# Kernel optimization log

Hardware: AMD Instinct MI355X
Metric: run time of the kernel (lower is better)

The kernel has to match this reference:

```python
import jax, jax.numpy as jnp
import numpy as np

N = 16384          # tokens
D_IN = 512         # input_dim
D_OUT = 512        # output_dim
H = 256            # expert hidden
E = 10             # num_experts
TOP_K = 2


def setup_inputs() -> dict:
    key = jax.random.key(0)
    ks = jax.random.split(key, 12)
    s_in = 1.0 / np.sqrt(D_IN)
    s_h = 1.0 / np.sqrt(H)
    s_o = 1.0 / np.sqrt(D_OUT)
    return {
        "x": jax.random.normal(ks[0], (N, D_IN), dtype=jnp.float32),
        "gate_w": jax.random.uniform(ks[1], (D_IN, E), minval=-s_in, maxval=s_in),
        "gate_b": jax.random.uniform(ks[2], (E,), minval=-s_in, maxval=s_in),
        "w1": jax.random.uniform(ks[3], (E, D_IN, H), minval=-s_in, maxval=s_in),
        "b1": jax.random.uniform(ks[4], (E, H), minval=-s_in, maxval=s_in),
        "w2": jax.random.uniform(ks[5], (E, H, D_OUT), minval=-s_h, maxval=s_h),
        "b2": jax.random.uniform(ks[6], (E, D_OUT), minval=-s_h, maxval=s_h),
        "cls_w": jax.random.uniform(ks[7], (D_OUT, D_OUT), minval=-s_o, maxval=s_o),
        "cls_b": jax.random.uniform(ks[8], (D_OUT,), minval=-s_o, maxval=s_o),
        "vec_w": jax.random.uniform(ks[9], (D_OUT, D_OUT), minval=-s_o, maxval=s_o),
        "vec_b": jax.random.uniform(ks[10], (D_OUT,), minval=-s_o, maxval=s_o),
    }


def reference(x, gate_w, gate_b, w1, b1, w2, b2, cls_w, cls_b, vec_w, vec_b):
    # Gating: softmax over experts, take top-k, renormalize
    gate_probs = jax.nn.softmax(x @ gate_w + gate_b, axis=-1)          # [N, E]
    top_v, top_i = jax.lax.top_k(gate_probs, TOP_K)                    # [N, K]
    top_v = top_v / jnp.sum(top_v, axis=-1, keepdims=True)
    # Scatter renormalized top-k probs into dense per-expert weights [N, E]
    n_idx = jnp.arange(x.shape[0])[:, None]
    w = jnp.zeros_like(gate_probs).at[n_idx, top_i].add(top_v)
    # Expert MLPs (vectorized over experts; zero weight == not dispatched)
    h = jax.nn.relu(jnp.einsum("nd,edh->neh", x, w1) + b1)             # [N, E, H]
    y = jnp.einsum("neh,eho->neo", h, w2) + b2                          # [N, E, Dout]
    combined = jnp.einsum("neo,ne->no", y, w)                           # [N, Dout]
    cls_out = combined @ cls_w + cls_b
    vec_out = combined @ vec_w + vec_b
    return (cls_out, vec_out)
```

## Files before the change

### kernel.cpp

```cpp
#include <hip/hip_runtime.h>

#define NTOK 16384
#define DIN  512
#define DOUT 512
#define HDIM 256
#define NEXP 10
#define NSLOT (2*NTOK)
#define NSEG  (2*NEXP)
#define BM 128
#define BN 128
#define BK 64

typedef unsigned short u16;
typedef unsigned int   u32;
typedef short s16x8 __attribute__((ext_vector_type(8)));
typedef float f32x4 __attribute__((ext_vector_type(4)));

__device__ __forceinline__ u16 f2b(float f){
  union { float f; u32 u; } c; c.f = f;
  u32 r = c.u + 0x7FFFu + ((c.u >> 16) & 1u);
  return (u16)(r >> 16);
}
__device__ __forceinline__ float b2f(u16 v){
  union { u32 u; float f; } c; c.u = ((u32)v) << 16; return c.f;
}
__device__ __forceinline__ u32 pk2(float lo, float hi){
  return (u32)f2b(lo) | ((u32)f2b(hi) << 16);
}
__device__ __forceinline__ s16x8 cvt8(const float* p){
  f32x4 a = *(const f32x4*)p;
  f32x4 b = *(const f32x4*)(p + 4);
  s16x8 r;
  r[0]=(short)f2b(a[0]); r[1]=(short)f2b(a[1]); r[2]=(short)f2b(a[2]); r[3]=(short)f2b(a[3]);
  r[4]=(short)f2b(b[0]); r[5]=(short)f2b(b[1]); r[6]=(short)f2b(b[2]); r[7]=(short)f2b(b[3]);
  return r;
}

__global__ __launch_bounds__(64) void k_zero(int* counts){
  if (threadIdx.x < NSEG) counts[threadIdx.x] = 0;
}

__global__ __launch_bounds__(256) void k_gate(
    const float* __restrict__ x, const float* __restrict__ gw, const float* __restrict__ gb,
    int* __restrict__ tke, float* __restrict__ tkw, int* __restrict__ counts)
{
  __shared__ int cnt[NSEG];
  if (threadIdx.x < NSEG) cnt[threadIdx.x] = 0;
  __syncthreads();
  const int wave = threadIdx.x >> 6, lane = threadIdx.x & 63;
  const int token = blockIdx.x * 4 + wave;
  float acc[NEXP];
  #pragma unroll
  for (int e = 0; e < NEXP; ++e) acc[e] = 0.f;
  const float* xr = x + (size_t)token * DIN;
  #pragma unroll
  for (int i = 0; i < DIN/64; ++i){
    int d = lane + 64*i;
    float xv = xr[d];
    const float* g = gw + (size_t)d * NEXP;
    #pragma unroll
    for (int e = 0; e < NEXP; ++e) acc[e] += xv * g[e];
  }
  #pragma unroll
  for (int e = 0; e < NEXP; ++e){
    #pragma unroll
    for (int off = 32; off > 0; off >>= 1) acc[e] += __shfl_xor(acc[e], off, 64);
  }
  if (lane == 0){
    float l[NEXP];
    #pragma unroll
    for (int e = 0; e < NEXP; ++e) l[e] = acc[e] + gb[e];
    int bi = 0; float bv = l[0];
    #pragma unroll
    for (int e = 1; e < NEXP; ++e) if (l[e] > bv){ bv = l[e]; bi = e; }
    int si = -1; float sv = -1e30f;
    #pragma unroll
    for (int e = 0; e < NEXP; ++e) if (e != bi && l[e] > sv){ sv = l[e]; si = e; }
    float w0 = 1.f / (1.f + expf(sv - bv));
    tke[2*token]   = bi;  tke[2*token+1] = si;
    tkw[2*token]   = w0;  tkw[2*token+1] = 1.f - w0;
    atomicAdd(&cnt[2*bi], 1);  atomicAdd(&cnt[2*si+1], 1);
  }
  __syncthreads();
  if (threadIdx.x < NSEG && cnt[threadIdx.x] > 0)
    atomicAdd(&counts[threadIdx.x], cnt[threadIdx.x]);
}

__global__ __launch_bounds__(64) void k_scan(
    const int* __restrict__ counts, int* __restrict__ offsets, int* __restrict__ cursors)
{
  if (threadIdx.x == 0){
    int s = 0;
    for (int i = 0; i < NSEG; ++i){ offsets[i] = s; s += counts[i]; }
    offsets[NSEG] = s;
  }
  if (threadIdx.x < NSEG) cursors[threadIdx.x] = 0;
}

__global__ __launch_bounds__(256) void k_scatter(
    const int* __restrict__ tke, const float* __restrict__ tkw,
    const int* __restrict__ offsets, int* __restrict__ cursors,
    int* __restrict__ tok_slot, float* __restrict__ w_slot)
{
  __shared__ int lcnt[NSEG], lbase[NSEG];
  if (threadIdx.x < NSEG) lcnt[threadIdx.x] = 0;
  __syncthreads();
  int n = blockIdx.x * 256 + threadIdx.x;
  int g0 = 2*tke[2*n], g1 = 2*tke[2*n+1] + 1;
  int p0 = atomicAdd(&lcnt[g0], 1);
  int p1 = atomicAdd(&lcnt[g1], 1);
  __syncthreads();
  if (threadIdx.x < NSEG) lbase[threadIdx.x] = atomicAdd(&cursors[threadIdx.x], lcnt[threadIdx.x]);
  __syncthreads();
  int s0 = offsets[g0] + lbase[g0] + p0;
  int s1 = offsets[g1] + lbase[g1] + p1;
  tok_slot[s0] = n; w_slot[s0] = tkw[2*n];
  tok_slot[s1] = n; w_slot[s1] = tkw[2*n+1];
}

__global__ __launch_bounds__(256) void k_wt(
    const float* __restrict__ in, u16* __restrict__ out, int R, int C)
{
  __shared__ float tile[32][33];
  const float* src = in + (size_t)blockIdx.z * R * C;
  u16* dst = out + (size_t)blockIdx.z * R * C;
  int cb = blockIdx.x * 32, rb = blockIdx.y * 32;
  int tx = threadIdx.x & 31, ty = threadIdx.x >> 5;
  #pragma unroll
  for (int i = 0; i < 4; ++i)
    tile[ty + i*8][tx] = src[(size_t)(rb + ty + i*8) * C + cb + tx];
  __syncthreads();
  #pragma unroll
  for (int i = 0; i < 4; ++i)
    dst[(size_t)(cb + ty + i*8) * R + rb + tx] = f2b(tile[tx][ty + i*8]);
}

__global__ __launch_bounds__(256, 2) void k_h(
    const float* __restrict__ x, const u16* __restrict__ w1tb, const float* __restrict__ b1,
    const int* __restrict__ offsets, const int* __restrict__ tok_slot,
    u16* __restrict__ h)
{
  __shared__ __align__(16) char pool[65536];
  u16* As = (u16*)pool;
  u16* Bs = (u16*)(pool + 32768);
  __shared__ int toks[BM];
  const int e   = blockIdx.z;
  const int off = offsets[2*e];
  const int cnt = offsets[2*e+2] - off;
  const int c0  = blockIdx.x * BM;
  if (c0 >= cnt) return;
  const int n0  = blockIdx.y * BN;
  const int tid = threadIdx.x;

  if (tid < BM){
    int r = c0 + tid;
    toks[tid] = tok_slot[off + (r < cnt ? r : cnt - 1)];
  }
  __syncthreads();

  const u16* Bg = w1tb + ((size_t)e * HDIM + n0) * DIN;

  int crow[4], ckk[4];
  #pragma unroll
  for (int i = 0; i < 4; ++i){
    int c = tid + i*256;
    crow[i] = c >> 3; ckk[i] = (c & 7) * 8;
  }
  int tokr[4];
  #pragma unroll
  for (int i = 0; i < 4; ++i) tokr[i] = toks[crow[i]];

  s16x8 ra[4], rb[4];
  auto loadregs = [&](int ks){
    #pragma unroll
    for (int i = 0; i < 4; ++i){
      ra[i] = cvt8(x + (size_t)tokr[i]*DIN + ks*BK + ckk[i]);
      rb[i] = *(const s16x8*)(Bg + (size_t)crow[i]*DIN + ks*BK + ckk[i]);
    }
  };
  auto writeregs = [&](int buf){
    #pragma unroll
    for (int i = 0; i < 4; ++i){
      u32 byt = (u32)((crow[i]*BK + ckk[i])*2) ^ ((u32)(crow[i]&7)<<4);
      *(s16x8*)((char*)As + buf*16384 + byt) = ra[i];
      *(s16x8*)((char*)Bs + buf*16384 + byt) = rb[i];
    }
  };

  const int wv = tid >> 6, lane = tid & 63;
  const int lr = lane & 15, lk = lane >> 4;
  const int wr = (wv >> 1) * 64, wc = (wv & 1) * 64;

  f32x4 acc[4][4];
  #pragma unroll
  for (int i = 0; i < 4; ++i)
    #pragma unroll
    for (int j = 0; j < 4; ++j) acc[i][j] = (f32x4){0.f,0.f,0.f,0.f};

  loadregs(0); writeregs(0);
  int cur = 0;
  const int NK = DIN / BK;
  for (int ks = 0; ks < NK; ++ks){
    __syncthreads();
    if (ks + 1 < NK) loadregs(ks + 1);
    #pragma unroll
    for (int sub = 0; sub < 2; ++sub){
      s16x8 af[4], bf[4];
      #pragma unroll
      for (int g = 0; g < 4; ++g){
        int arow = wr + g*16 + lr;
        u32 ab = (u32)((arow*BK + sub*32 + lk*8)*2) ^ ((u32)(arow&7)<<4);
        af[g] = *(const s16x8*)((char*)As + cur*16384 + ab);
        int bcol = wc + g*16 + lr;
        u32 bb = (u32)((bcol*BK + sub*32 + lk*8)*2) ^ ((u32)(bcol&7)<<4);
        bf[g] = *(const s16x8*)((char*)Bs + cur*16384 + bb);
      }
      #pragma unroll
      for (int i = 0; i < 4; ++i)
        #pragma unroll
        for (int j = 0; j < 4; ++j)
          acc[i][j] = __builtin_amdgcn_mfma_f32_16x16x32_bf16(af[i], bf[j], acc[i][j], 0, 0, 0);
    }
    if (ks + 1 < NK) writeregs(cur ^ 1);
    cur ^= 1;
  }
  __syncthreads();

  u16* outh = (u16*)pool;
  #pragma unroll
  for (int j = 0; j < 4; ++j){
    int col = wc + j*16 + lr;
    float bias = b1[e*HDIM + n0 + col];
    #pragma unroll
    for (int i = 0; i < 4; ++i)
      #pragma unroll
      for (int r = 0; r < 4; ++r){
        int row = wr + i*16 + lk*4 + r;
        float v = acc[i][j][r] + bias;
        outh[row*136 + col] = f2b(v > 0.f ? v : 0.f);
      }
  }
  __syncthreads();
  {
    int r = tid >> 1, half = tid & 1;
    if (c0 + r < cnt){
      u16* dst = h + (size_t)(off + c0 + r) * HDIM + n0 + half*64;
      const u16* src = outh + r*136 + half*64;
      #pragma unroll
      for (int q = 0; q < 8; ++q)
        *(s16x8*)(dst + q*8) = *(const s16x8*)(src + q*8);
    }
  }
}

template<int PASS>
__global__ __launch_bounds__(256, 2) void k_y(
    const u16* __restrict__ h, const u16* __restrict__ w2tb, const float* __restrict__ b2,
    const int* __restrict__ offsets, const int* __restrict__ tok_slot,
    const float* __restrict__ w_slot, u16* __restrict__ cmb)
{
  __shared__ __align__(16) char pool[67584];
  u16* As = (u16*)pool;
  u16* Bs = (u16*)(pool + 32768);
  __shared__ int   toks[BM];
  __shared__ float wts[BM];
  const int e    = blockIdx.z;
  const int segb = offsets[2*e + PASS];
  const int segc = offsets[2*e + PASS + 1] - segb;
  const int c0   = blockIdx.x * BM;
  if (c0 >= segc) return;
  const int n0   = blockIdx.y * BN;
  const int tid  = threadIdx.x;

  if (tid < BM){
    int r = c0 + tid;
    int s = segb + (r < segc ? r : segc - 1);
    toks[tid] = tok_slot[s];
    wts[tid]  = w_slot[s];
  }

  const u16* Ag = h + (size_t)(segb + c0) * HDIM;
  const u16* Bg = w2tb + ((size_t)e * DOUT + n0) * HDIM;

  int crow[4], ckk[4];
  #pragma unroll
  for (int i = 0; i < 4; ++i){
    int c = tid + i*256;
    crow[i] = c >> 3; ckk[i] = (c & 7) * 8;
  }
  s16x8 ra[4], rb[4];
  auto loadregs = [&](int ks){
    #pragma unroll
    for (int i = 0; i < 4; ++i){
      ra[i] = *(const s16x8*)(Ag + (size_t)crow[i]*HDIM + ks*BK + ckk[i]);
      rb[i] = *(const s16x8*)(Bg + (size_t)crow[i]*HDIM + ks*BK + ckk[i]);
    }
  };
  auto writeregs = [&](int buf){
    #pragma unroll
    for (int i = 0; i < 4; ++i){
      u32 byt = (u32)((crow[i]*BK + ckk[i])*2) ^ ((u32)(crow[i]&7)<<4);
      *(s16x8*)((char*)As + buf*16384 + byt) = ra[i];
      *(s16x8*)((char*)Bs + buf*16384 + byt) = rb[i];
    }
  };

  const int wv = tid >> 6, lane = tid & 63;
  const int lr = lane & 15, lk = lane >> 4;
  const int wr = (wv >> 1) * 64, wc = (wv & 1) * 64;

  f32x4 acc[4][4];
  #pragma unroll
  for (int i = 0; i < 4; ++i)
    #pragma unroll
    for (int j = 0; j < 4; ++j) acc[i][j] = (f32x4){0.f,0.f,0.f,0.f};

  loadregs(0); writeregs(0);
  int cur = 0;
  const int NK = HDIM / BK;
  for (int ks = 0; ks < NK; ++ks){
    __syncthreads();
    if (ks + 1 < NK) loadregs(ks + 1);
    #pragma unroll
    for (int sub = 0; sub < 2; ++sub){
      s16x8 af[4], bf[4];
      #pragma unroll
      for (int g = 0; g < 4; ++g){
        int arow = wr + g*16 + lr;
        u32 ab = (u32)((arow*BK + sub*32 + lk*8)*2) ^ ((u32)(arow&7)<<4);
        af[g] = *(const s16x8*)((char*)As + cur*16384 + ab);
        int bcol = wc + g*16 + lr;
        u32 bb = (u32)((bcol*BK + sub*32 + lk*8)*2) ^ ((u32)(bcol&7)<<4);
        bf[g] = *(const s16x8*)((char*)Bs + cur*16384 + bb);
      }
      #pragma unroll
      for (int i = 0; i < 4; ++i)
        #pragma unroll
        for (int j = 0; j < 4; ++j)
          acc[i][j] = __builtin_amdgcn_mfma_f32_16x16x32_bf16(af[i], bf[j], acc[i][j], 0, 0, 0);
    }
    if (ks + 1 < NK) writeregs(cur ^ 1);
    cur ^= 1;
  }
  __syncthreads();

  float* outf = (float*)pool;
  #pragma unroll
  for (int j = 0; j < 4; ++j){
    int col = wc + j*16 + lr;
    float bias = b2[e*DOUT + n0 + col];
    #pragma unroll
    for (int i = 0; i < 4; ++i)
      #pragma unroll
      for (int r = 0; r < 4; ++r){
        int row = wr + i*16 + lk*4 + r;
        outf[row*132 + col] = wts[row] * (acc[i][j][r] + bias);
      }
  }
  __syncthreads();
  {
    int r = tid >> 1, half = tid & 1;
    if (c0 + r < segc){
      u16* dst = cmb + (size_t)toks[r] * 1024 + n0 + half*64;
      const float* src = outf + r*132 + half*64;
      #pragma unroll
      for (int q = 0; q < 8; ++q){
        s16x8 o;
        if (PASS == 0){
          #pragma unroll
          for (int m = 0; m < 8; ++m) o[m] = (short)f2b(src[q*8 + m]);
        } else {
          s16x8 old = *(const s16x8*)(dst + q*8);
          #pragma unroll
          for (int m = 0; m < 8; ++m)
            o[m] = (short)f2b(b2f((u16)old[m]) + src[q*8 + m]);
        }
        *(s16x8*)(dst + q*8) = o;
      }
    }
  }
}

__global__ __launch_bounds__(512, 4) void k_cls(
    const u16* __restrict__ cmb, const float* __restrict__ W,
    const float* __restrict__ bias, float* __restrict__ out)
{
  __shared__ __align__(16) char Bs[2][10240];
  const int tid = threadIdx.x;
  const int r0  = blockIdx.x * 256;
  const int c0  = blockIdx.y * 128;

  const int bc4 = tid >> 4;
  const int bkp = tid & 15;
  u32 bpk[4];
  auto loadB = [&](int ks){
    const float* p0 = W + (size_t)(ks*32 + 2*bkp) * DOUT + c0 + bc4*4;
    f32x4 v0 = *(const f32x4*)p0;
    f32x4 v1 = *(const f32x4*)(p0 + DOUT);
    #pragma unroll
    for (int m = 0; m < 4; ++m) bpk[m] = pk2(v0[m], v1[m]);
  };
  auto writeB = [&](int buf){
    #pragma unroll
    for (int m = 0; m < 4; ++m)
      *(u32*)(Bs[buf] + (bc4*4 + m)*80 + bkp*4) = bpk[m];
  };

  const int wv = tid >> 6, lane = tid & 63;
  const int lr = lane & 15, lk = lane >> 4;
  const int rg = wv >> 1, cg = wv & 1;
  const u16* Arow = cmb + (size_t)(r0 + rg*64) * 1024;

  f32x4 acc[4][4];
  #pragma unroll
  for (int i = 0; i < 4; ++i)
    #pragma unroll
    for (int j = 0; j < 4; ++j) acc[i][j] = (f32x4){0.f,0.f,0.f,0.f};

  s16x8 af[4], afn[4];
  auto loadA = [&](s16x8* a, int ks){
    #pragma unroll
    for (int g = 0; g < 4; ++g)
      a[g] = *(const s16x8*)(Arow + (size_t)(g*16 + lr)*1024 + ks*32 + lk*8);
  };

  loadB(0); writeB(0); loadA(af, 0);
  int cur = 0;
  for (int ks = 0; ks < 16; ++ks){
    __syncthreads();
    if (ks + 1 < 16){ loadB(ks + 1); loadA(afn, ks + 1); }
    s16x8 bf[4];
    #pragma unroll
    for (int j = 0; j < 4; ++j)
      bf[j] = *(const s16x8*)(Bs[cur] + (cg*64 + j*16 + lr)*80 + lk*16);
    #pragma unroll
    for (int i = 0; i < 4; ++i)
      #pragma unroll
      for (int j = 0; j < 4; ++j)
        acc[i][j] = __builtin_amdgcn_mfma_f32_16x16x32_bf16(af[i], bf[j], acc[i][j], 0, 0, 0);
    if (ks + 1 < 16) writeB(cur ^ 1);
    #pragma unroll
    for (int g = 0; g < 4; ++g) af[g] = afn[g];
    cur ^= 1;
  }

  #pragma unroll
  for (int j = 0; j < 4; ++j){
    int col = c0 + cg*64 + j*16 + lr;
    float bv = bias[col];
    #pragma unroll
    for (int i = 0; i < 4; ++i)
      #pragma unroll
      for (int r = 0; r < 4; ++r){
        int row = r0 + rg*64 + i*16 + lk*4 + r;
        out[(size_t)row * DOUT + col] = acc[i][j][r] + bv;
      }
  }
}

__global__ __launch_bounds__(512, 2) void k_vip(
    const float* __restrict__ W, const float* __restrict__ bias,
    u16* __restrict__ cmbio)
{
  __shared__ __align__(16) char Bs[2][40960];
  const int tid = threadIdx.x;
  const int r0  = blockIdx.x * 64;

  int bc4[4], bkp[4];
  #pragma unroll
  for (int u = 0; u < 4; ++u){
    int idx = tid + u*512;
    bc4[u] = idx >> 4;
    bkp[u] = idx & 15;
  }
  u32 bpk[4][4];
  auto loadB = [&](int ks){
    #pragma unroll
    for (int u = 0; u < 4; ++u){
      const float* p0 = W + (size_t)(ks*32 + 2*bkp[u]) * DOUT + bc4[u]*4;
      f32x4 v0 = *(const f32x4*)p0;
      f32x4 v1 = *(const f32x4*)(p0 + DOUT);
      #pragma unroll
      for (int m = 0; m < 4; ++m) bpk[u][m] = pk2(v0[m], v1[m]);
    }
  };
  auto writeB = [&](int buf){
    #pragma unroll
    for (int u = 0; u < 4; ++u)
      #pragma unroll
      for (int m = 0; m < 4; ++m)
        *(u32*)(Bs[buf] + (bc4[u]*4 + m)*80 + bkp[u]*4) = bpk[u][m];
  };

  const int wv = tid >> 6, lane = tid & 63;
  const int lr = lane & 15, lk = lane >> 4;
  const int wc = wv * 64;
  const u16* Arow = cmbio + (size_t)r0 * 1024;

  f32x4 acc[4][4];
  #pragma unroll
  for (int i = 0; i < 4; ++i)
    #pragma unroll
    for (int j = 0; j < 4; ++j) acc[i][j] = (f32x4){0.f,0.f,0.f,0.f};

  s16x8 af[4], afn[4];
  auto loadA = [&](s16x8* a, int ks){
    #pragma unroll
    for (int g = 0; g < 4; ++g)
      a[g] = *(const s16x8*)(Arow + (size_t)(g*16 + lr)*1024 + ks*32 + lk*8);
  };

  loadB(0); writeB(0); loadA(af, 0);
  int cur = 0;
  for (int ks = 0; ks < 16; ++ks){
    __syncthreads();
    if (ks + 1 < 16){ loadB(ks + 1); loadA(afn, ks + 1); }
    s16x8 bf[4];
    #pragma unroll
    for (int g = 0; g < 4; ++g)
      bf[g] = *(const s16x8*)(Bs[cur] + (wc + g*16 + lr)*80 + lk*16);
    #pragma unroll
    for (int i = 0; i < 4; ++i)
      #pragma unroll
      for (int j = 0; j < 4; ++j)
        acc[i][j] = __builtin_amdgcn_mfma_f32_16x16x32_bf16(af[i], bf[j], acc[i][j], 0, 0, 0);
    if (ks + 1 < 16) writeB(cur ^ 1);
    #pragma unroll
    for (int g = 0; g < 4; ++g) af[g] = afn[g];
    cur ^= 1;
  }
  __syncthreads();

  float* out = (float*)cmbio;
  #pragma unroll
  for (int j = 0; j < 4; ++j){
    int col = wc + j*16 + lr;
    float bv = bias[col];
    #pragma unroll
    for (int i = 0; i < 4; ++i)
      #pragma unroll
      for (int r = 0; r < 4; ++r){
        int row = r0 + i*16 + lk*4 + r;
        out[(size_t)row * DOUT + col] = acc[i][j][r] + bv;
      }
  }
}

extern "C" void kernel_launch(void* const* d_in, const int* in_sizes, int n_in,
                              void* d_out, int out_size, void* d_ws, size_t ws_size,
                              hipStream_t stream)
{
  const float* x    = (const float*)d_in[0];
  const float* gw   = (const float*)d_in[1];
  const float* gb   = (const float*)d_in[2];
  const float* w1   = (const float*)d_in[3];
  const float* b1   = (const float*)d_in[4];
  const float* w2   = (const float*)d_in[5];
  const float* b2   = (const float*)d_in[6];
  const float* clsw = (const float*)d_in[7];
  const float* clsb = (const float*)d_in[8];
  const float* vecw = (const float*)d_in[9];
  const float* vecb = (const float*)d_in[10];

  char* base = (char*)d_out;
  float* cls_out  = (float*)base;
  u16*   cmb      = (u16*)(base + ((size_t)32<<20));
  u16*   h        = (u16*)base;
  char*  mb       = base + ((size_t)16<<20) + (128<<10);
  int*   tok_slot = (int*)  mb;
  float* w_slot   = (float*)(mb + 131072);
  int*   tke      = (int*)  (mb + 262144);
  float* tkw      = (float*)(mb + 393216);
  int*   counts   = (int*)  (mb + 524288);
  int*   offsets  = (int*)  (mb + 524544);
  int*   cursors  = (int*)  (mb + 524800);
  u16*   w1tb     = (u16*)(base + ((size_t)18<<20));
  u16*   w2tb     = (u16*)(base + ((size_t)21<<20));

  k_zero<<<dim3(1), dim3(64), 0, stream>>>(counts);
  k_gate<<<dim3(NTOK/4), dim3(256), 0, stream>>>(x, gw, gb, tke, tkw, counts);
  k_scan<<<dim3(1), dim3(64), 0, stream>>>(counts, offsets, cursors);
  k_scatter<<<dim3(NTOK/256), dim3(256), 0, stream>>>(tke, tkw, offsets, cursors,
                                                      tok_slot, w_slot);
  k_wt<<<dim3(HDIM/32, DIN/32, NEXP), dim3(256), 0, stream>>>(w1, w1tb, DIN, HDIM);
  k_wt<<<dim3(DOUT/32, HDIM/32, NEXP), dim3(256), 0, stream>>>(w2, w2tb, HDIM, DOUT);
  k_h<<<dim3(256, 2, NEXP), dim3(256), 0, stream>>>(x, w1tb, b1, offsets, tok_slot, h);
  k_y<0><<<dim3(128, 4, NEXP), dim3(256), 0, stream>>>(h, w2tb, b2, offsets, tok_slot, w_slot, cmb);
  k_y<1><<<dim3(128, 4, NEXP), dim3(256), 0, stream>>>(h, w2tb, b2, offsets, tok_slot, w_slot, cmb);
  k_cls<<<dim3(NTOK/256, DOUT/128), dim3(512), 0, stream>>>(cmb, clsw, clsb, cls_out);
  k_vip<<<dim3(NTOK/64), dim3(512), 0, stream>>>(vecw, vecb, cmb);
}
```

Measured before the change: 252.2 us.

## Pretranspose vec weights into workspace and use hardware bf16 pack conversion

Converts fp32 to bf16 with the v_cvt_pk_bf16_f32 instruction instead of manual bit rounding. When the workspace holds at least 1 MB, the vec_w matrix is pre-transposed into bf16 there. A new in-place kernel then reads its B fragments straight from global memory with no LDS staging, 32 rows per block. The goal is to cut conversion ALU work and the in-kernel weight conversion and LDS traffic in the final projection. The cost is an extra transpose launch and uncached, uncoalesced-ish global B loads.

```diff
diff --git a/kernel.cpp b/kernel.cpp
--- a/kernel.cpp
+++ b/kernel.cpp
@@ -25,15 +25,17 @@
   union { u32 u; float f; } c; c.u = ((u32)v) << 16; return c.f;
 }
 __device__ __forceinline__ u32 pk2(float lo, float hi){
-  return (u32)f2b(lo) | ((u32)f2b(hi) << 16);
+  u32 r;
+  asm("v_cvt_pk_bf16_f32 %0, %1, %2" : "=v"(r) : "v"(lo), "v"(hi));
+  return r;
 }
 __device__ __forceinline__ s16x8 cvt8(const float* p){
   f32x4 a = *(const f32x4*)p;
   f32x4 b = *(const f32x4*)(p + 4);
-  s16x8 r;
-  r[0]=(short)f2b(a[0]); r[1]=(short)f2b(a[1]); r[2]=(short)f2b(a[2]); r[3]=(short)f2b(a[3]);
-  r[4]=(short)f2b(b[0]); r[5]=(short)f2b(b[1]); r[6]=(short)f2b(b[2]); r[7]=(short)f2b(b[3]);
-  return r;
+  union { u32 u[4]; s16x8 v; } c;
+  c.u[0] = pk2(a[0], a[1]); c.u[1] = pk2(a[2], a[3]);
+  c.u[2] = pk2(b[0], b[1]); c.u[3] = pk2(b[2], b[3]);
+  return c.v;
 }
 
 __global__ __launch_bounds__(64) void k_zero(int* counts){
@@ -538,6 +540,53 @@
     float bv = bias[col];
     #pragma unroll
     for (int i = 0; i < 4; ++i)
+      #pragma unroll
+      for (int r = 0; r < 4; ++r){
+        int row = r0 + i*16 + lk*4 + r;
+        out[(size_t)row * DOUT + col] = acc[i][j][r] + bv;
+      }
+  }
+}
+
+__global__ __launch_bounds__(256, 4) void k_vipw(
+    const u16* __restrict__ wT, const float* __restrict__ bias,
+    u16* __restrict__ cmbio)
+{
+  const int tid = threadIdx.x;
+  const int r0  = blockIdx.x * 32;
+  const int wv = tid >> 6, lane = tid & 63;
+  const int lr = lane & 15, lk = lane >> 4;
+  const int wc = wv * 128;
+  const u16* Arow = cmbio + (size_t)r0 * 1024;
+
+  f32x4 acc[2][8];
+  #pragma unroll
+  for (int i = 0; i < 2; ++i)
+    #pragma unroll
+    for (int j = 0; j < 8; ++j) acc[i][j] = (f32x4){0.f,0.f,0.f,0.f};
+
+  for (int ks = 0; ks < 16; ++ks){
+    s16x8 af[2];
+    #pragma unroll
+    for (int g = 0; g < 2; ++g)
+      af[g] = *(const s16x8*)(Arow + (size_t)(g*16 + lr)*1024 + ks*32 + lk*8);
+    #pragma unroll
+    for (int j = 0; j < 8; ++j){
+      s16x8 bf = *(const s16x8*)(wT + (size_t)(wc + j*16 + lr)*DOUT + ks*32 + lk*8);
+      #pragma unroll
+      for (int i = 0; i < 2; ++i)
+        acc[i][j] = __builtin_amdgcn_mfma_f32_16x16x32_bf16(af[i], bf, acc[i][j], 0, 0, 0);
+    }
+  }
+  __syncthreads();
+
+  float* out = (float*)cmbio;
+  #pragma unroll
+  for (int j = 0; j < 8; ++j){
+    int col = wc + j*16 + lr;
+    float bv = bias[col];
+    #pragma unroll
+    for (int i = 0; i < 2; ++i)
       #pragma unroll
       for (int r = 0; r < 4; ++r){
         int row = r0 + i*16 + lk*4 + r;
@@ -577,6 +626,9 @@
   u16*   w1tb     = (u16*)(base + ((size_t)18<<20));
   u16*   w2tb     = (u16*)(base + ((size_t)21<<20));
 
+  const bool usews = (ws_size >= (size_t)(1<<20));
+  u16* vecwT = (u16*)d_ws;
+
   k_zero<<<dim3(1), dim3(64), 0, stream>>>(counts);
   k_gate<<<dim3(NTOK/4), dim3(256), 0, stream>>>(x, gw, gb, tke, tkw, counts);
   k_scan<<<dim3(1), dim3(64), 0, stream>>>(counts, offsets, cursors);
@@ -584,9 +636,14 @@
                                                       tok_slot, w_slot);
   k_wt<<<dim3(HDIM/32, DIN/32, NEXP), dim3(256), 0, stream>>>(w1, w1tb, DIN, HDIM);
   k_wt<<<dim3(DOUT/32, HDIM/32, NEXP), dim3(256), 0, stream>>>(w2, w2tb, HDIM, DOUT);
+  if (usews)
+    k_wt<<<dim3(DOUT/32, DIN/32, 1), dim3(256), 0, stream>>>(vecw, vecwT, DOUT, DOUT);
   k_h<<<dim3(256, 2, NEXP), dim3(256), 0, stream>>>(x, w1tb, b1, offsets, tok_slot, h);
   k_y<0><<<dim3(128, 4, NEXP), dim3(256), 0, stream>>>(h, w2tb, b2, offsets, tok_slot, w_slot, cmb);
   k_y<1><<<dim3(128, 4, NEXP), dim3(256), 0, stream>>>(h, w2tb, b2, offsets, tok_slot, w_slot, cmb);
   k_cls<<<dim3(NTOK/256, DOUT/128), dim3(512), 0, stream>>>(cmb, clsw, clsb, cls_out);
-  k_vip<<<dim3(NTOK/64), dim3(512), 0, stream>>>(vecw, vecb, cmb);
-}
+  if (usews)
+    k_vipw<<<dim3(NTOK/32), dim3(256), 0, stream>>>(vecwT, vecb, cmb);
+  else
+    k_vip<<<dim3(NTOK/64), dim3(512), 0, stream>>>(vecw, vecb, cmb);
+}
```

Result: faster. 242.3 us (-3.9%).
